# Kernel optimization log

Measured on AMD Instinct MI355X. Metric: run time of the kernel, lower is better.

## Reference

```python
import jax, jax.numpy as jnp
import numpy as np
from jax import lax

V, D, L, H, MAXLEN = 32000, 512, 6, 8, 1024
DH = D // H
DFF = 4 * D
B, T = 8, 1024


def _ln(x, g, b, eps=1e-5):
    m = jnp.mean(x, axis=-1, keepdims=True)
    v = jnp.var(x, axis=-1, keepdims=True)
    return (x - m) * lax.rsqrt(v + eps) * g + b


def setup_inputs() -> dict:
    key = jax.random.key(0)
    ks = jax.random.split(key, 16)
    s = 0.02
    inp = {
        "idx": jax.random.randint(ks[0], (B, T), 0, V, dtype=jnp.int32),
        "wte": jax.random.normal(ks[1], (V, D), jnp.float32) * s,   # tied with head
        "wpe": jax.random.normal(ks[2], (MAXLEN, D), jnp.float32) * s,
        # per-layer stacked params [L, ...]
        "ln1_g": jnp.ones((L, D), jnp.float32),
        "ln1_b": jnp.zeros((L, D), jnp.float32),
        "w_qkv": jax.random.normal(ks[3], (L, D, 3 * D), jnp.float32) * s,
        "b_qkv": jnp.zeros((L, 3 * D), jnp.float32),
        "w_ao": jax.random.normal(ks[4], (L, D, D), jnp.float32) * s,
        "b_ao": jnp.zeros((L, D), jnp.float32),
        "ln2_g": jnp.ones((L, D), jnp.float32),
        "ln2_b": jnp.zeros((L, D), jnp.float32),
        "w_fc": jax.random.normal(ks[5], (L, D, DFF), jnp.float32) * s,
        "b_fc": jnp.zeros((L, DFF), jnp.float32),
        "w_pr": jax.random.normal(ks[6], (L, DFF, D), jnp.float32) * s,
        "b_pr": jnp.zeros((L, D), jnp.float32),
        "lnf_g": jnp.ones((D,), jnp.float32),
        "lnf_b": jnp.zeros((D,), jnp.float32),
    }
    return inp


def reference(idx, wte, wpe, ln1_g, ln1_b, w_qkv, b_qkv, w_ao, b_ao,
              ln2_g, ln2_b, w_fc, b_fc, w_pr, b_pr, lnf_g, lnf_b):
    Bx, Tx = idx.shape
    x = wte[idx] + wpe[:Tx]                      # [B,T,D]
    causal = jnp.tril(jnp.ones((Tx, Tx), bool))  # [T,T]
    scale = 1.0 / np.sqrt(DH)

    def block(x, p):
        (g1, b1, wqkv, bqkv, wao, bao, g2, b2, wfc, bfc, wpr, bpr) = p
        h = _ln(x, g1, b1)
        qkv = h @ wqkv + bqkv                    # [B,T,3D]
        q, k, v = jnp.split(qkv, 3, axis=-1)
        q = q.reshape(Bx, Tx, H, DH)
        k = k.reshape(Bx, Tx, H, DH)
        v = v.reshape(Bx, Tx, H, DH)
        att = jnp.einsum('bqhd,bkhd->bhqk', q, k) * scale
        att = jnp.where(causal, att, -jnp.inf)
        att = jax.nn.softmax(att, axis=-1)
        y = jnp.einsum('bhqk,bkhd->bqhd', att, v).reshape(Bx, Tx, D)
        x = x + y @ wao + bao
        h = _ln(x, g2, b2)
        h = jax.nn.gelu(h @ wfc + bfc, approximate=False)
        x = x + h @ wpr + bpr
        return x, None

    params = (ln1_g, ln1_b, w_qkv, b_qkv, w_ao, b_ao,
              ln2_g, ln2_b, w_fc, b_fc, w_pr, b_pr)
    x, _ = lax.scan(block, x, params)
    x = _ln(x, lnf_g, lnf_b)
    logits = x @ wte.T                           # tied head, [B,T,V]
    return logits
```

## Files before the change

kernel.cpp:

```cpp
#include <hip/hip_runtime.h>
#include <hip/hip_bf16.h>
#include <math.h>

#define V_   32000
#define D_   512
#define L_   6
#define H_   8
#define DH_  64
#define DFF_ 2048
#define B_   8
#define T_   1024
#define BT_  (B_*T_)

typedef __attribute__((ext_vector_type(4))) float f32x4;
typedef __attribute__((ext_vector_type(8))) short short8;
using bf16_t = __hip_bfloat16;

__device__ __forceinline__ float b2f(unsigned short u) {
    union { unsigned int i; float f; } v; v.i = ((unsigned int)u) << 16; return v.f;
}
__device__ __forceinline__ unsigned short f2b(float f) {
    bf16_t h = __float2bfloat16(f);
    return *reinterpret_cast<unsigned short*>(&h);
}
__device__ __forceinline__ void gl16(const void* g, void* l) {
    __builtin_amdgcn_global_load_lds((const __attribute__((address_space(1))) void*)g,
                                     (__attribute__((address_space(3))) void*)l, 16, 0, 0);
}
__device__ __forceinline__ float gelu_exact(float v) {
    return 0.5f * v * (1.0f + erff(v * 0.70710678118654752f));
}

__global__ __launch_bounds__(128) void embed_kernel(
        const int* __restrict__ idx, const float* __restrict__ wte,
        const float* __restrict__ wpe, float* __restrict__ x) {
    int bt = blockIdx.x;
    int t  = bt & (T_ - 1);
    int tok = idx[bt];
    const float4* wr = (const float4*)(wte + (size_t)tok * D_);
    const float4* pr = (const float4*)(wpe + (size_t)t * D_);
    float4* xr = (float4*)(x + (size_t)bt * D_);
    int i = threadIdx.x;
    float4 a = wr[i], b = pr[i];
    xr[i] = make_float4(a.x + b.x, a.y + b.y, a.z + b.z, a.w + b.w);
}

__global__ __launch_bounds__(128) void ln_kernel(
        const float* __restrict__ x, const float* __restrict__ g,
        const float* __restrict__ b, bf16_t* __restrict__ out) {
    int bt = blockIdx.x;
    int i  = threadIdx.x;
    float4 v = ((const float4*)(x + (size_t)bt * D_))[i];
    float s  = v.x + v.y + v.z + v.w;
    float sq = v.x*v.x + v.y*v.y + v.z*v.z + v.w*v.w;
    #pragma unroll
    for (int o = 32; o > 0; o >>= 1) {
        s  += __shfl_down(s,  o);
        sq += __shfl_down(sq, o);
    }
    __shared__ float ss[2], ssq[2];
    if ((i & 63) == 0) { ss[i >> 6] = s; ssq[i >> 6] = sq; }
    __syncthreads();
    float mean = (ss[0] + ss[1]) * (1.0f / D_);
    float var  = (ssq[0] + ssq[1]) * (1.0f / D_) - mean * mean;
    float rstd = rsqrtf(var + 1e-5f);
    float4 gg = ((const float4*)g)[i];
    float4 bb = ((const float4*)b)[i];
    ushort4 o4;
    o4.x = f2b((v.x - mean) * rstd * gg.x + bb.x);
    o4.y = f2b((v.y - mean) * rstd * gg.y + bb.y);
    o4.z = f2b((v.z - mean) * rstd * gg.z + bb.z);
    o4.w = f2b((v.w - mean) * rstd * gg.w + bb.w);
    ((ushort4*)(out + (size_t)bt * D_))[i] = o4;
}

__global__ __launch_bounds__(256) void conv_kernel(
        const float* __restrict__ s, bf16_t* __restrict__ d, int n4) {
    int i = blockIdx.x * 256 + threadIdx.x;
    if (i >= n4) return;
    float4 f = ((const float4*)s)[i];
    ushort4 u = make_ushort4(f2b(f.x), f2b(f.y), f2b(f.z), f2b(f.w));
    ((ushort4*)d)[i] = u;
}

__global__ __launch_bounds__(256) void tconv_kernel(
        const float* __restrict__ src, bf16_t* __restrict__ dst, int K, int N) {
    size_t ls = (size_t)K * N;
    const float* s = src + blockIdx.z * ls;
    bf16_t* d = dst + blockIdx.z * ls;
    __shared__ float tile[32][33];
    int n0 = blockIdx.x * 32, k0 = blockIdx.y * 32;
    int c = threadIdx.x & 31, r8 = threadIdx.x >> 5;
    #pragma unroll
    for (int i = 0; i < 4; ++i) {
        int r = r8 + i * 8;
        tile[r][c] = s[(size_t)(k0 + r) * N + n0 + c];
    }
    __syncthreads();
    #pragma unroll
    for (int i = 0; i < 4; ++i) {
        int r = r8 + i * 8;
        d[(size_t)(n0 + r) * K + k0 + c] = __float2bfloat16(tile[c][r]);
    }
}

template<int ACT, bool OBF, bool RES, bool CONVB>
__global__ __launch_bounds__(256) void mm_kernel(
        const bf16_t* __restrict__ A,
        const bf16_t* __restrict__ Bt,
        const float*  __restrict__ Bf,
        const float*  __restrict__ bias,
        const float*  __restrict__ res,
        void* __restrict__ Cout,
        int M, int N, int K)
{
    __shared__ __align__(16) unsigned short As[128 * 64];
    __shared__ __align__(16) unsigned short Bs[128 * 64];
    const int nwg = gridDim.x;
    const int orig = blockIdx.x;
    const int q8 = nwg >> 3, r8 = nwg & 7;
    const int xcd = orig & 7, lin = orig >> 3;
    const int wg = (xcd < r8) ? xcd * (q8 + 1) + lin
                              : r8 * (q8 + 1) + (xcd - r8) * q8 + lin;
    const int gym = M >> 7;
    const int by = wg % gym;
    const int bx = wg / gym;

    const int t    = threadIdx.x;
    const int row0 = by * 128;
    const int col0 = bx * 128;
    const int lane = t & 63;
    const int wid  = t >> 6;
    const int wm   = (wid & 1) * 64;
    const int wn   = (wid >> 1) * 64;
    const int fr   = lane & 15;
    const int fq   = lane >> 4;

    f32x4 acc[4][4];
    #pragma unroll
    for (int m = 0; m < 4; ++m)
        #pragma unroll
        for (int n = 0; n < 4; ++n)
            acc[m][n] = (f32x4)(0.0f);

    const unsigned short* Ab  = (const unsigned short*)A;
    const unsigned short* Btb = (const unsigned short*)Bt;

    for (int k0 = 0; k0 < K; k0 += 64) {
        __syncthreads();
        #pragma unroll
        for (int i = 0; i < 4; ++i) {
            int c = t + i * 256;
            int row = c >> 3;
            int sl  = (c & 7) ^ (row & 7);
            gl16(Ab + (size_t)(row0 + row) * K + k0 + sl * 8, As + (size_t)c * 8);
        }
        if (!CONVB) {
            #pragma unroll
            for (int i = 0; i < 4; ++i) {
                int c = t + i * 256;
                int row = c >> 3;
                int sl  = (c & 7) ^ (row & 7);
                gl16(Btb + (size_t)(col0 + row) * K + k0 + sl * 8, Bs + (size_t)c * 8);
            }
        } else {
            #pragma unroll
            for (int i = 0; i < 4; ++i) {
                int c = t + i * 256;
                int row = c >> 3;
                int sl  = (c & 7) ^ (row & 7);
                const float* sp = Bf + (size_t)(col0 + row) * K + k0 + sl * 8;
                float4 f0 = ((const float4*)sp)[0];
                float4 f1 = ((const float4*)sp)[1];
                short8 pk;
                pk[0] = f2b(f0.x); pk[1] = f2b(f0.y); pk[2] = f2b(f0.z); pk[3] = f2b(f0.w);
                pk[4] = f2b(f1.x); pk[5] = f2b(f1.y); pk[6] = f2b(f1.z); pk[7] = f2b(f1.w);
                *(short8*)(Bs + (size_t)c * 8) = pk;
            }
        }
        __syncthreads();

        #pragma unroll
        for (int kk = 0; kk < 2; ++kk) {
            short8 av[4], bv[4];
            #pragma unroll
            for (int m = 0; m < 4; ++m) {
                int R = wm + m * 16 + fr;
                int sl = (kk * 4 + fq) ^ (fr & 7);
                av[m] = *(const short8*)(As + (size_t)R * 64 + sl * 8);
            }
            #pragma unroll
            for (int n = 0; n < 4; ++n) {
                int R = wn + n * 16 + fr;
                int sl = (kk * 4 + fq) ^ (fr & 7);
                bv[n] = *(const short8*)(Bs + (size_t)R * 64 + sl * 8);
            }
            #pragma unroll
            for (int m = 0; m < 4; ++m)
                #pragma unroll
                for (int n = 0; n < 4; ++n)
                    acc[m][n] = __builtin_amdgcn_mfma_f32_16x16x32_bf16(av[m], bv[n], acc[m][n], 0, 0, 0);
        }
    }

    #pragma unroll
    for (int n = 0; n < 4; ++n) {
        int col = col0 + wn + n * 16 + fr;
        float bb = bias ? bias[col] : 0.0f;
        #pragma unroll
        for (int m = 0; m < 4; ++m) {
            int rbase = row0 + wm + m * 16 + fq * 4;
            #pragma unroll
            for (int r = 0; r < 4; ++r) {
                float v = acc[m][n][r] + bb;
                if (ACT == 1) v = gelu_exact(v);
                size_t off = (size_t)(rbase + r) * N + col;
                if (RES) v += res[off];
                if (OBF) ((bf16_t*)Cout)[off] = __float2bfloat16(v);
                else     ((float*)Cout)[off]  = v;
            }
        }
    }
}

__global__ __launch_bounds__(512, 2) void flash_kernel(
        const bf16_t* __restrict__ qkv, bf16_t* __restrict__ y)
{
    __shared__ __align__(16) unsigned short Ks[64][72];
    __shared__ __align__(16) unsigned short Vt[64][72];
    __shared__ __align__(16) unsigned short Pls[128][72];

    const int qt = (T_ / 128 - 1) - (blockIdx.x >> 6);
    const int bh = blockIdx.x & 63;
    const int h  = bh & (H_ - 1);
    const int b  = bh >> 3;
    const int t  = threadIdx.x;
    const int lane = t & 63;
    const int w    = t >> 6;
    const int fr   = lane & 15;
    const int fq   = lane >> 4;

    const unsigned short* qkvb = (const unsigned short*)qkv;

    short8 avq[2];
    {
        const unsigned short* qrow = qkvb +
            (size_t)(b * T_ + qt * 128 + w * 16 + fr) * (3 * D_) + h * DH_;
        avq[0] = *(const short8*)(qrow + fq * 8);
        avq[1] = *(const short8*)(qrow + 32 + fq * 8);
    }

    float mi[4], li[4];
    f32x4 oacc[4];
    #pragma unroll
    for (int r = 0; r < 4; ++r) { mi[r] = -INFINITY; li[r] = 0.0f; }
    #pragma unroll
    for (int d = 0; d < 4; ++d) oacc[d] = (f32x4)(0.0f);

    const int nt = 2 * qt + 2;
    for (int jt = 0; jt < nt; ++jt) {
        __syncthreads();
        {
            int j = t >> 3, seg = t & 7;
            const unsigned short* kr = qkvb +
                (size_t)(b * T_ + jt * 64 + j) * (3 * D_) + D_ + h * DH_ + seg * 8;
            *(short8*)&Ks[j][seg * 8] = *(const short8*)kr;
            short8 vv = *(const short8*)(kr + D_);
            int dbase = seg * 8;
            Vt[dbase + 0][j] = vv[0]; Vt[dbase + 1][j] = vv[1];
            Vt[dbase + 2][j] = vv[2]; Vt[dbase + 3][j] = vv[3];
            Vt[dbase + 4][j] = vv[4]; Vt[dbase + 5][j] = vv[5];
            Vt[dbase + 6][j] = vv[6]; Vt[dbase + 7][j] = vv[7];
        }
        __syncthreads();

        f32x4 s[4];
        #pragma unroll
        for (int jb = 0; jb < 4; ++jb) s[jb] = (f32x4)(0.0f);
        #pragma unroll
        for (int ks = 0; ks < 2; ++ks) {
            #pragma unroll
            for (int jb = 0; jb < 4; ++jb) {
                short8 bv = *(const short8*)(&Ks[jb * 16 + fr][ks * 32 + fq * 8]);
                s[jb] = __builtin_amdgcn_mfma_f32_16x16x32_bf16(avq[ks], bv, s[jb], 0, 0, 0);
            }
        }

        float sv[4][4];
        const int qgb = qt * 128 + w * 16 + fq * 4;
        #pragma unroll
        for (int jb = 0; jb < 4; ++jb) {
            int jg = jt * 64 + jb * 16 + fr;
            #pragma unroll
            for (int r = 0; r < 4; ++r) {
                float x = s[jb][r] * 0.125f;
                sv[jb][r] = (jg > qgb + r) ? -INFINITY : x;
            }
        }

        #pragma unroll
        for (int r = 0; r < 4; ++r) {
            float tm = fmaxf(fmaxf(sv[0][r], sv[1][r]), fmaxf(sv[2][r], sv[3][r]));
            tm = fmaxf(tm, __shfl_xor(tm, 1));
            tm = fmaxf(tm, __shfl_xor(tm, 2));
            tm = fmaxf(tm, __shfl_xor(tm, 4));
            tm = fmaxf(tm, __shfl_xor(tm, 8));
            float mnew = fmaxf(mi[r], tm);
            float corr = __expf(mi[r] - mnew);
            float tsum = 0.0f;
            #pragma unroll
            for (int jb = 0; jb < 4; ++jb) {
                float p = __expf(sv[jb][r] - mnew);
                sv[jb][r] = p;
                tsum += p;
            }
            tsum += __shfl_xor(tsum, 1);
            tsum += __shfl_xor(tsum, 2);
            tsum += __shfl_xor(tsum, 4);
            tsum += __shfl_xor(tsum, 8);
            li[r] = li[r] * corr + tsum;
            mi[r] = mnew;
            #pragma unroll
            for (int db = 0; db < 4; ++db) oacc[db][r] *= corr;
        }

        #pragma unroll
        for (int jb = 0; jb < 4; ++jb)
            #pragma unroll
            for (int r = 0; r < 4; ++r)
                Pls[w * 16 + fq * 4 + r][jb * 16 + fr] = f2b(sv[jb][r]);

        #pragma unroll
        for (int ks = 0; ks < 2; ++ks) {
            short8 ap = *(const short8*)(&Pls[w * 16 + fr][ks * 32 + fq * 8]);
            #pragma unroll
            for (int db = 0; db < 4; ++db) {
                short8 bv = *(const short8*)(&Vt[db * 16 + fr][ks * 32 + fq * 8]);
                oacc[db] = __builtin_amdgcn_mfma_f32_16x16x32_bf16(ap, bv, oacc[db], 0, 0, 0);
            }
        }
    }

    unsigned short* yb = (unsigned short*)y;
    #pragma unroll
    for (int r = 0; r < 4; ++r) {
        float inv = 1.0f / li[r];
        size_t row = (size_t)(b * T_ + qt * 128 + w * 16 + fq * 4 + r);
        #pragma unroll
        for (int db = 0; db < 4; ++db)
            yb[row * D_ + h * DH_ + db * 16 + fr] = f2b(oacc[db][r] * inv);
    }
}

extern "C" void kernel_launch(void* const* d_in, const int* in_sizes, int n_in,
                              void* d_out, int out_size, void* d_ws, size_t ws_size,
                              hipStream_t stream) {
    const int*   idx   = (const int*)  d_in[0];
    const float* wte   = (const float*)d_in[1];
    const float* wpe   = (const float*)d_in[2];
    const float* ln1_g = (const float*)d_in[3];
    const float* ln1_b = (const float*)d_in[4];
    const float* w_qkv = (const float*)d_in[5];
    const float* b_qkv = (const float*)d_in[6];
    const float* w_ao  = (const float*)d_in[7];
    const float* b_ao  = (const float*)d_in[8];
    const float* ln2_g = (const float*)d_in[9];
    const float* ln2_b = (const float*)d_in[10];
    const float* w_fc  = (const float*)d_in[11];
    const float* b_fc  = (const float*)d_in[12];
    const float* w_pr  = (const float*)d_in[13];
    const float* b_pr  = (const float*)d_in[14];
    const float* lnf_g = (const float*)d_in[15];
    const float* lnf_b = (const float*)d_in[16];
    float* outf = (float*)d_out;

    char* base = (char*)d_out;
    size_t off = 0;
    auto alloc = [&](size_t bytes) {
        void* p = base + off;
        off += (bytes + 255) & ~(size_t)255;
        return p;
    };
    bf16_t* wqkvT = (bf16_t*)alloc((size_t)L_ * 3 * D_ * D_ * 2);
    bf16_t* waoT  = (bf16_t*)alloc((size_t)L_ * D_ * D_ * 2);
    bf16_t* wfcT  = (bf16_t*)alloc((size_t)L_ * DFF_ * D_ * 2);
    bf16_t* wprT  = (bf16_t*)alloc((size_t)L_ * D_ * DFF_ * 2);
    bf16_t* qkvb  = (bf16_t*)alloc((size_t)BT_ * 3 * D_ * 2);
    bf16_t* yb    = (bf16_t*)alloc((size_t)BT_ * D_ * 2);
    bf16_t* hab   = (bf16_t*)alloc((size_t)BT_ * D_ * 2);
    bf16_t* fcb   = (bf16_t*)alloc((size_t)BT_ * DFF_ * 2);
    float*  xb    = (float*) alloc((size_t)BT_ * D_ * 4);

    bf16_t* hfin = (bf16_t*)d_ws;
    size_t hbytes = ((size_t)BT_ * D_ * 2 + 255) & ~(size_t)255;
    bool wte_ws = ws_size >= hbytes + (size_t)V_ * D_ * 2 + 256;
    bf16_t* wteb = wte_ws ? (bf16_t*)((char*)d_ws + hbytes) : nullptr;

    if (wte_ws)
        conv_kernel<<<(V_ * D_ / 4 + 255) / 256, 256, 0, stream>>>(wte, wteb, V_ * D_ / 4);
    tconv_kernel<<<dim3(3 * D_ / 32, D_ / 32, L_), 256, 0, stream>>>(w_qkv, wqkvT, D_, 3 * D_);
    tconv_kernel<<<dim3(D_ / 32, D_ / 32, L_), 256, 0, stream>>>(w_ao, waoT, D_, D_);
    tconv_kernel<<<dim3(DFF_ / 32, D_ / 32, L_), 256, 0, stream>>>(w_fc, wfcT, D_, DFF_);
    tconv_kernel<<<dim3(D_ / 32, DFF_ / 32, L_), 256, 0, stream>>>(w_pr, wprT, DFF_, D_);

    embed_kernel<<<BT_, 128, 0, stream>>>(idx, wte, wpe, xb);

    for (int l = 0; l < L_; ++l) {
        ln_kernel<<<BT_, 128, 0, stream>>>(xb, ln1_g + l * D_, ln1_b + l * D_, hab);
        mm_kernel<0, true, false, false><<<12 * 64, 256, 0, stream>>>(
            hab, wqkvT + (size_t)l * 3 * D_ * D_, nullptr, b_qkv + (size_t)l * 3 * D_,
            nullptr, qkvb, BT_, 3 * D_, D_);
        flash_kernel<<<512, 512, 0, stream>>>(qkvb, yb);
        mm_kernel<0, false, true, false><<<4 * 64, 256, 0, stream>>>(
            yb, waoT + (size_t)l * D_ * D_, nullptr, b_ao + (size_t)l * D_,
            xb, xb, BT_, D_, D_);
        ln_kernel<<<BT_, 128, 0, stream>>>(xb, ln2_g + l * D_, ln2_b + l * D_, hab);
        mm_kernel<1, true, false, false><<<16 * 64, 256, 0, stream>>>(
            hab, wfcT + (size_t)l * DFF_ * D_, nullptr, b_fc + (size_t)l * DFF_,
            nullptr, fcb, BT_, DFF_, D_);
        mm_kernel<0, false, true, false><<<4 * 64, 256, 0, stream>>>(
            fcb, wprT + (size_t)l * D_ * DFF_, nullptr, b_pr + (size_t)l * D_,
            xb, xb, BT_, D_, DFF_);
    }

    ln_kernel<<<BT_, 128, 0, stream>>>(xb, lnf_g, lnf_b, hfin);
    if (wte_ws)
        mm_kernel<0, false, false, false><<<250 * 64, 256, 0, stream>>>(
            hfin, wteb, nullptr, nullptr, nullptr, outf, BT_, V_, D_);
    else
        mm_kernel<0, false, false, true><<<250 * 64, 256, 0, stream>>>(
            hfin, nullptr, wte, nullptr, nullptr, outf, BT_, V_, D_);
}
```

Before: 1.797 ms.

## Split-K the narrow projection GEMMs and fuse partial reduction with residual and LayerNorm

The attention-output and MLP-down projections, which launched only 256 workgroups, now run split-K (2 and 4 splits) and write fp32 partial sums to a scratch buffer. A new reduce_ln kernel sums the partials, adds bias and residual, writes the residual stream, and applies the next LayerNorm, replacing the separate ln_kernel launches. This aims to fill more compute units on the narrow N=512 GEMMs and remove standalone LayerNorm passes. In exchange it adds extra fp32 partial-sum traffic, up to four BT×D buffers per layer.

```diff
diff --git a/kernel.cpp b/kernel.cpp
--- a/kernel.cpp
+++ b/kernel.cpp
@@ -74,6 +74,51 @@
     ((ushort4*)(out + (size_t)bt * D_))[i] = o4;
 }
 
+template<int S>
+__global__ __launch_bounds__(128) void reduce_ln_kernel(
+        const float* __restrict__ part,
+        const float* __restrict__ bias,
+        const float* __restrict__ xin,
+        float*       __restrict__ xout,
+        const float* __restrict__ g, const float* __restrict__ bb,
+        bf16_t*      __restrict__ hout)
+{
+    int bt = blockIdx.x;
+    int i  = threadIdx.x;
+    size_t rowo = (size_t)bt * D_ + i * 4;
+    float4 v  = *(const float4*)(xin + rowo);
+    float4 bv = ((const float4*)bias)[i];
+    v.x += bv.x; v.y += bv.y; v.z += bv.z; v.w += bv.w;
+    #pragma unroll
+    for (int s = 0; s < S; ++s) {
+        float4 p = *(const float4*)(part + (size_t)s * BT_ * D_ + rowo);
+        v.x += p.x; v.y += p.y; v.z += p.z; v.w += p.w;
+    }
+    *(float4*)(xout + rowo) = v;
+
+    float su  = v.x + v.y + v.z + v.w;
+    float sq = v.x*v.x + v.y*v.y + v.z*v.z + v.w*v.w;
+    #pragma unroll
+    for (int o = 32; o > 0; o >>= 1) {
+        su += __shfl_down(su, o);
+        sq += __shfl_down(sq, o);
+    }
+    __shared__ float ss[2], ssq[2];
+    if ((i & 63) == 0) { ss[i >> 6] = su; ssq[i >> 6] = sq; }
+    __syncthreads();
+    float mean = (ss[0] + ss[1]) * (1.0f / D_);
+    float var  = (ssq[0] + ssq[1]) * (1.0f / D_) - mean * mean;
+    float rstd = rsqrtf(var + 1e-5f);
+    float4 gg = ((const float4*)g)[i];
+    float4 b2 = ((const float4*)bb)[i];
+    ushort4 o4;
+    o4.x = f2b((v.x - mean) * rstd * gg.x + b2.x);
+    o4.y = f2b((v.y - mean) * rstd * gg.y + b2.y);
+    o4.z = f2b((v.z - mean) * rstd * gg.z + b2.z);
+    o4.w = f2b((v.w - mean) * rstd * gg.w + b2.w);
+    ((ushort4*)(hout + (size_t)bt * D_))[i] = o4;
+}
+
 __global__ __launch_bounds__(256) void conv_kernel(
         const float* __restrict__ s, bf16_t* __restrict__ d, int n4) {
     int i = blockIdx.x * 256 + threadIdx.x;
@@ -104,7 +149,7 @@
     }
 }
 
-template<int ACT, bool OBF, bool RES, bool CONVB>
+template<int ACT, bool OBF, bool RES, bool CONVB, bool SPLIT>
 __global__ __launch_bounds__(256) void mm_kernel(
         const bf16_t* __restrict__ A,
         const bf16_t* __restrict__ Bt,
@@ -112,7 +157,7 @@
         const float*  __restrict__ bias,
         const float*  __restrict__ res,
         void* __restrict__ Cout,
-        int M, int N, int K)
+        int M, int N, int K, int S)
 {
     __shared__ __align__(16) unsigned short As[128 * 64];
     __shared__ __align__(16) unsigned short Bs[128 * 64];
@@ -123,8 +168,11 @@
     const int wg = (xcd < r8) ? xcd * (q8 + 1) + lin
                               : r8 * (q8 + 1) + (xcd - r8) * q8 + lin;
     const int gym = M >> 7;
-    const int by = wg % gym;
-    const int bx = wg / gym;
+    const int tiles = gym * (N >> 7);
+    const int ks  = SPLIT ? (wg / tiles) : 0;
+    const int rem = SPLIT ? (wg % tiles) : wg;
+    const int by = rem % gym;
+    const int bx = rem / gym;
 
     const int t    = threadIdx.x;
     const int row0 = by * 128;
@@ -146,7 +194,9 @@
     const unsigned short* Ab  = (const unsigned short*)A;
     const unsigned short* Btb = (const unsigned short*)Bt;
 
-    for (int k0 = 0; k0 < K; k0 += 64) {
+    const int Kc   = SPLIT ? (K / S) : K;
+    const int kbeg = ks * Kc;
+    for (int k0 = kbeg; k0 < kbeg + Kc; k0 += 64) {
         __syncthreads();
         #pragma unroll
         for (int i = 0; i < 4; ++i) {
@@ -201,6 +251,22 @@
                 for (int n = 0; n < 4; ++n)
                     acc[m][n] = __builtin_amdgcn_mfma_f32_16x16x32_bf16(av[m], bv[n], acc[m][n], 0, 0, 0);
         }
+    }
+
+    if (SPLIT) {
+        float* P = (float*)Cout + (size_t)ks * M * N;
+        #pragma unroll
+        for (int n = 0; n < 4; ++n) {
+            int col = col0 + wn + n * 16 + fr;
+            #pragma unroll
+            for (int m = 0; m < 4; ++m) {
+                int rbase = row0 + wm + m * 16 + fq * 4;
+                #pragma unroll
+                for (int r = 0; r < 4; ++r)
+                    P[(size_t)(rbase + r) * N + col] = acc[m][n][r];
+            }
+        }
+        return;
     }
 
     #pragma unroll
@@ -390,6 +456,7 @@
     bf16_t* hab   = (bf16_t*)alloc((size_t)BT_ * D_ * 2);
     bf16_t* fcb   = (bf16_t*)alloc((size_t)BT_ * DFF_ * 2);
     float*  xb    = (float*) alloc((size_t)BT_ * D_ * 4);
+    float*  psum  = (float*) alloc((size_t)4 * BT_ * D_ * 4);
 
     bf16_t* hfin = (bf16_t*)d_ws;
     size_t hbytes = ((size_t)BT_ * D_ * 2 + 255) & ~(size_t)255;
@@ -404,30 +471,38 @@
     tconv_kernel<<<dim3(D_ / 32, DFF_ / 32, L_), 256, 0, stream>>>(w_pr, wprT, DFF_, D_);
 
     embed_kernel<<<BT_, 128, 0, stream>>>(idx, wte, wpe, xb);
+    ln_kernel<<<BT_, 128, 0, stream>>>(xb, ln1_g, ln1_b, hab);
 
     for (int l = 0; l < L_; ++l) {
-        ln_kernel<<<BT_, 128, 0, stream>>>(xb, ln1_g + l * D_, ln1_b + l * D_, hab);
-        mm_kernel<0, true, false, false><<<12 * 64, 256, 0, stream>>>(
+        mm_kernel<0, true, false, false, false><<<12 * 64, 256, 0, stream>>>(
             hab, wqkvT + (size_t)l * 3 * D_ * D_, nullptr, b_qkv + (size_t)l * 3 * D_,
-            nullptr, qkvb, BT_, 3 * D_, D_);
+            nullptr, qkvb, BT_, 3 * D_, D_, 1);
         flash_kernel<<<512, 512, 0, stream>>>(qkvb, yb);
-        mm_kernel<0, false, true, false><<<4 * 64, 256, 0, stream>>>(
-            yb, waoT + (size_t)l * D_ * D_, nullptr, b_ao + (size_t)l * D_,
-            xb, xb, BT_, D_, D_);
-        ln_kernel<<<BT_, 128, 0, stream>>>(xb, ln2_g + l * D_, ln2_b + l * D_, hab);
-        mm_kernel<1, true, false, false><<<16 * 64, 256, 0, stream>>>(
+        mm_kernel<0, false, false, false, true><<<4 * 64 * 2, 256, 0, stream>>>(
+            yb, waoT + (size_t)l * D_ * D_, nullptr, nullptr,
+            nullptr, psum, BT_, D_, D_, 2);
+        reduce_ln_kernel<2><<<BT_, 128, 0, stream>>>(
+            psum, b_ao + (size_t)l * D_, xb, xb,
+            ln2_g + (size_t)l * D_, ln2_b + (size_t)l * D_, hab);
+        mm_kernel<1, true, false, false, false><<<16 * 64, 256, 0, stream>>>(
             hab, wfcT + (size_t)l * DFF_ * D_, nullptr, b_fc + (size_t)l * DFF_,
-            nullptr, fcb, BT_, DFF_, D_);
-        mm_kernel<0, false, true, false><<<4 * 64, 256, 0, stream>>>(
-            fcb, wprT + (size_t)l * D_ * DFF_, nullptr, b_pr + (size_t)l * D_,
-            xb, xb, BT_, D_, DFF_);
-    }
-
-    ln_kernel<<<BT_, 128, 0, stream>>>(xb, lnf_g, lnf_b, hfin);
+            nullptr, fcb, BT_, DFF_, D_, 1);
+        mm_kernel<0, false, false, false, true><<<4 * 64 * 4, 256, 0, stream>>>(
+            fcb, wprT + (size_t)l * D_ * DFF_, nullptr, nullptr,
+            nullptr, psum, BT_, D_, DFF_, 4);
+        if (l < L_ - 1)
+            reduce_ln_kernel<4><<<BT_, 128, 0, stream>>>(
+                psum, b_pr + (size_t)l * D_, xb, xb,
+                ln1_g + (size_t)(l + 1) * D_, ln1_b + (size_t)(l + 1) * D_, hab);
+        else
+            reduce_ln_kernel<4><<<BT_, 128, 0, stream>>>(
+                psum, b_pr + (size_t)l * D_, xb, xb, lnf_g, lnf_b, hfin);
+    }
+
     if (wte_ws)
-        mm_kernel<0, false, false, false><<<250 * 64, 256, 0, stream>>>(
-            hfin, wteb, nullptr, nullptr, nullptr, outf, BT_, V_, D_);
+        mm_kernel<0, false, false, false, false><<<250 * 64, 256, 0, stream>>>(
+            hfin, wteb, nullptr, nullptr, nullptr, outf, BT_, V_, D_, 1);
     else
-        mm_kernel<0, false, false, true><<<250 * 64, 256, 0, stream>>>(
-            hfin, nullptr, wte, nullptr, nullptr, outf, BT_, V_, D_);
-}
+        mm_kernel<0, false, false, true, false><<<250 * 64, 256, 0, stream>>>(
+            hfin, nullptr, wte, nullptr, nullptr, outf, BT_, V_, D_, 1);
+}
```

Result: no change. 1.820 ms (+1.3%).

## Add 256x256-tile 8-wave GEMM with phased prefetch for QKV, FC and LM head

Applied to the files above, without the earlier changes.

Adds a new GEMM kernel that uses 256x256 output tiles with 512 threads. It double-buffers K-slices in LDS using swizzled direct-to-LDS loads split into four compute phases, raises wave priority around the MFMA bursts, and remaps workgroups so consecutive tiles share an XCD. It replaces the older 128-tile kernel for the QKV projection, the FC+GELU projection and the vocab head. The goal is more operand reuse per LDS byte and better L2 locality. In exchange it uses much more LDS and more registers per workgroup, and the residual projections are left unchanged.

```diff
diff --git a/kernel.cpp b/kernel.cpp
--- a/kernel.cpp
+++ b/kernel.cpp
@@ -223,6 +223,140 @@
     }
 }
 
+#define MM8_PHASE(MH, NH, HALF, SRCB, R0, DSTB)                               \
+  {                                                                           \
+    short8 af[2][4]; short8 bg[2][2];                                         \
+    _Pragma("unroll")                                                         \
+    for (int ks = 0; ks < 2; ++ks) {                                          \
+      _Pragma("unroll")                                                       \
+      for (int m = 0; m < 4; ++m) {                                           \
+        int row = ((MH)*4 + m)*32 + wm*16 + fr;                               \
+        int sl  = (ks*4 + fq) ^ (fr & 7);                                     \
+        af[ks][m] = *(const short8*)(curA + (size_t)row*64 + (size_t)sl*8);   \
+      }                                                                       \
+      _Pragma("unroll")                                                       \
+      for (int n = 0; n < 2; ++n) {                                           \
+        int col = ((NH)*2 + n)*64 + wn*16 + fr;                               \
+        int sl  = (ks*4 + fq) ^ (fr & 7);                                     \
+        bg[ks][n] = *(const short8*)(curB + (size_t)col*64 + (size_t)sl*8);   \
+      }                                                                       \
+    }                                                                         \
+    if (pf) {                                                                 \
+      _Pragma("unroll")                                                       \
+      for (int i = 0; i < 2; ++i) {                                           \
+        int c = (HALF)*1024 + i*512 + t;                                      \
+        int row = c >> 3, sl = (c & 7) ^ (row & 7);                           \
+        gl16(SRCB + (size_t)((R0) + row)*K + k0n + sl*8,                      \
+             DSTB + (size_t)c*8);                                             \
+      }                                                                       \
+      asm volatile("s_waitcnt vmcnt(2)" ::: "memory");                        \
+    } else if ((MH) == 0 && (NH) == 0) {                                      \
+      asm volatile("s_waitcnt vmcnt(0)" ::: "memory");                        \
+    }                                                                         \
+    asm volatile("s_barrier" ::: "memory");                                   \
+    asm volatile("s_waitcnt lgkmcnt(0)" ::: "memory");                        \
+    __builtin_amdgcn_sched_barrier(0);                                        \
+    __builtin_amdgcn_s_setprio(1);                                            \
+    _Pragma("unroll")                                                         \
+    for (int ks = 0; ks < 2; ++ks)                                            \
+      _Pragma("unroll")                                                       \
+      for (int m = 0; m < 4; ++m)                                             \
+        _Pragma("unroll")                                                     \
+        for (int n = 0; n < 2; ++n)                                           \
+          acc[(MH)*4+m][(NH)*2+n] = __builtin_amdgcn_mfma_f32_16x16x32_bf16(  \
+              af[ks][m], bg[ks][n], acc[(MH)*4+m][(NH)*2+n], 0, 0, 0);        \
+    __builtin_amdgcn_s_setprio(0);                                            \
+    __builtin_amdgcn_sched_barrier(0);                                        \
+    asm volatile("s_barrier" ::: "memory");                                   \
+  }
+
+template<int ACT, bool OBF>
+__global__ __launch_bounds__(512) void mm8_kernel(
+        const bf16_t* __restrict__ A,
+        const bf16_t* __restrict__ Bt,
+        const float*  __restrict__ bias,
+        void* __restrict__ Cout,
+        int M, int N, int K)
+{
+    __shared__ __align__(16) unsigned short sA[2][256 * 64];
+    __shared__ __align__(16) unsigned short sB[2][256 * 64];
+
+    const int nwg = gridDim.x;
+    const int orig = blockIdx.x;
+    const int q8 = nwg >> 3, r8 = nwg & 7;
+    const int xcd = orig & 7, lin = orig >> 3;
+    const int wg = (xcd < r8) ? xcd * (q8 + 1) + lin
+                              : r8 * (q8 + 1) + (xcd - r8) * q8 + lin;
+    const int gym = M >> 8;
+    const int by = wg % gym;
+    const int bx = wg / gym;
+    const int row0 = by * 256;
+    const int col0 = bx * 256;
+
+    const int t    = threadIdx.x;
+    const int lane = t & 63;
+    const int wid  = t >> 6;
+    const int wm   = wid >> 2;
+    const int wn   = wid & 3;
+    const int fr   = lane & 15;
+    const int fq   = lane >> 4;
+
+    const unsigned short* Ab = (const unsigned short*)A;
+    const unsigned short* Bb = (const unsigned short*)Bt;
+
+    f32x4 acc[8][4];
+    #pragma unroll
+    for (int m = 0; m < 8; ++m)
+        #pragma unroll
+        for (int n = 0; n < 4; ++n)
+            acc[m][n] = (f32x4)(0.0f);
+
+    const int NK = K >> 6;
+
+    #pragma unroll
+    for (int h = 0; h < 2; ++h)
+        #pragma unroll
+        for (int i = 0; i < 2; ++i) {
+            int c = h * 1024 + i * 512 + t;
+            int row = c >> 3, sl = (c & 7) ^ (row & 7);
+            gl16(Ab + (size_t)(row0 + row) * K + sl * 8, &sA[0][(size_t)c * 8]);
+            gl16(Bb + (size_t)(col0 + row) * K + sl * 8, &sB[0][(size_t)c * 8]);
+        }
+    asm volatile("s_waitcnt vmcnt(0)" ::: "memory");
+    asm volatile("s_barrier" ::: "memory");
+
+    for (int s = 0; s < NK; ++s) {
+        const unsigned short* curA = sA[s & 1];
+        const unsigned short* curB = sB[s & 1];
+        unsigned short* nxA = (unsigned short*)sA[(s + 1) & 1];
+        unsigned short* nxB = (unsigned short*)sB[(s + 1) & 1];
+        const int k0n = (s + 1) << 6;
+        const bool pf = (s + 1) < NK;
+        MM8_PHASE(0, 0, 0, Ab, row0, nxA)
+        MM8_PHASE(1, 0, 0, Bb, col0, nxB)
+        MM8_PHASE(0, 1, 1, Ab, row0, nxA)
+        MM8_PHASE(1, 1, 1, Bb, col0, nxB)
+    }
+
+    #pragma unroll
+    for (int n = 0; n < 4; ++n) {
+        int col = col0 + n * 64 + wn * 16 + fr;
+        float bb = bias ? bias[col] : 0.0f;
+        #pragma unroll
+        for (int m = 0; m < 8; ++m) {
+            int rbase = row0 + m * 32 + wm * 16 + fq * 4;
+            #pragma unroll
+            for (int r = 0; r < 4; ++r) {
+                float v = acc[m][n][r] + bb;
+                if (ACT == 1) v = gelu_exact(v);
+                size_t off = (size_t)(rbase + r) * N + col;
+                if (OBF) ((bf16_t*)Cout)[off] = __float2bfloat16(v);
+                else     ((float*)Cout)[off]  = v;
+            }
+        }
+    }
+}
+
 __global__ __launch_bounds__(512, 2) void flash_kernel(
         const bf16_t* __restrict__ qkv, bf16_t* __restrict__ y)
 {
@@ -406,18 +540,18 @@
     embed_kernel<<<BT_, 128, 0, stream>>>(idx, wte, wpe, xb);
 
     for (int l = 0; l < L_; ++l) {
-        ln_kernel<<<BT_, 128, 0, stream>>>(xb, ln1_g + l * D_, ln1_b + l * D_, hab);
-        mm_kernel<0, true, false, false><<<12 * 64, 256, 0, stream>>>(
-            hab, wqkvT + (size_t)l * 3 * D_ * D_, nullptr, b_qkv + (size_t)l * 3 * D_,
-            nullptr, qkvb, BT_, 3 * D_, D_);
+        ln_kernel<<<BT_, 128, 0, stream>>>(xb, ln1_g + (size_t)l * D_, ln1_b + (size_t)l * D_, hab);
+        mm8_kernel<0, true><<<(BT_ / 256) * (3 * D_ / 256), 512, 0, stream>>>(
+            hab, wqkvT + (size_t)l * 3 * D_ * D_, b_qkv + (size_t)l * 3 * D_,
+            qkvb, BT_, 3 * D_, D_);
         flash_kernel<<<512, 512, 0, stream>>>(qkvb, yb);
         mm_kernel<0, false, true, false><<<4 * 64, 256, 0, stream>>>(
             yb, waoT + (size_t)l * D_ * D_, nullptr, b_ao + (size_t)l * D_,
             xb, xb, BT_, D_, D_);
-        ln_kernel<<<BT_, 128, 0, stream>>>(xb, ln2_g + l * D_, ln2_b + l * D_, hab);
-        mm_kernel<1, true, false, false><<<16 * 64, 256, 0, stream>>>(
-            hab, wfcT + (size_t)l * DFF_ * D_, nullptr, b_fc + (size_t)l * DFF_,
-            nullptr, fcb, BT_, DFF_, D_);
+        ln_kernel<<<BT_, 128, 0, stream>>>(xb, ln2_g + (size_t)l * D_, ln2_b + (size_t)l * D_, hab);
+        mm8_kernel<1, true><<<(BT_ / 256) * (DFF_ / 256), 512, 0, stream>>>(
+            hab, wfcT + (size_t)l * DFF_ * D_, b_fc + (size_t)l * DFF_,
+            fcb, BT_, DFF_, D_);
         mm_kernel<0, false, true, false><<<4 * 64, 256, 0, stream>>>(
             fcb, wprT + (size_t)l * D_ * DFF_, nullptr, b_pr + (size_t)l * D_,
             xb, xb, BT_, D_, DFF_);
@@ -425,8 +559,8 @@
 
     ln_kernel<<<BT_, 128, 0, stream>>>(xb, lnf_g, lnf_b, hfin);
     if (wte_ws)
-        mm_kernel<0, false, false, false><<<250 * 64, 256, 0, stream>>>(
-            hfin, wteb, nullptr, nullptr, nullptr, outf, BT_, V_, D_);
+        mm8_kernel<0, false><<<(BT_ / 256) * (V_ / 256), 512, 0, stream>>>(
+            hfin, wteb, nullptr, outf, BT_, V_, D_);
     else
         mm_kernel<0, false, false, true><<<250 * 64, 256, 0, stream>>>(
             hfin, nullptr, wte, nullptr, nullptr, outf, BT_, V_, D_);
```

Measured after the change: 1.724 ms. -4.1%, faster.
